# Optimization experiments

Hardware: AMD Instinct MI355X
Metric: run time of the kernel (lower is better)

## Reference

```python
import jax, jax.numpy as jnp
import numpy as np

BATCH = 8
N_CLASSES = 3            # including background
PRE_NMS_LIMIT = 6000
NMS_THRESH = 0.5
SCALE = 512.0
WINDOW = (0.0, 0.0, 512.0, 512.0)   # y1, x1, y2, x2
STD_DEV = np.array([0.1, 0.1, 0.2, 0.2], np.float32)
GROUP_OFFSET = 4096.0    # > image extent; separates (batch, class) groups in NMS

_RATIOS = np.array([0.5, 1.0, 2.0])
_LEVELS = [((128, 128), 4, 8.0), ((64, 64), 8, 16.0), ((32, 32), 16, 32.0), ((16, 16), 32, 64.0)]


def _gen_anchors():
    # faithful port of generate_pyramid_anchors / generate_anchors (anchor_stride=1)
    out = []
    for (fy, fx), stride, scale in _LEVELS:
        s, r = np.meshgrid(np.array([scale]), _RATIOS)
        s, r = s.flatten(), r.flatten()
        heights = s / np.sqrt(r)
        widths = s * np.sqrt(r)
        sy = np.arange(fy) * stride
        sx = np.arange(fx) * stride
        sx, sy = np.meshgrid(sx, sy)
        bw, bcx = np.meshgrid(widths, sx)
        bh, bcy = np.meshgrid(heights, sy)
        centers = np.stack([bcy, bcx], axis=2).reshape(-1, 2)
        sizes = np.stack([bh, bw], axis=2).reshape(-1, 2)
        out.append(np.concatenate([centers - 0.5 * sizes, centers + 0.5 * sizes], axis=1))
    return np.concatenate(out, axis=0).astype(np.float32)  # (65280, 4) yxyx


def setup_inputs() -> dict:
    key = jax.random.key(0)
    k1, k2 = jax.random.split(key)
    anchors = jnp.asarray(_gen_anchors())
    n_anchors = anchors.shape[0]
    n_prop = BATCH * n_anchors
    logits = jax.random.normal(k1, (n_prop, N_CLASSES), jnp.float32)
    probs = jax.nn.softmax(logits, axis=-1)
    deltas = jax.random.normal(k2, (n_prop, 4), jnp.float32)
    batch_ixs = jnp.repeat(jnp.arange(BATCH, dtype=jnp.int64), n_anchors)
    return {"probs": probs, "deltas": deltas, "anchors": anchors, "batch_ixs": batch_ixs}


def _apply_box_deltas_2d(boxes, deltas):
    # boxes: (K,4) yxyx (normalized); deltas: (K,4) dy,dx,dh,dw
    h = boxes[:, 2] - boxes[:, 0]
    w = boxes[:, 3] - boxes[:, 1]
    cy = boxes[:, 0] + 0.5 * h + deltas[:, 0] * h
    cx = boxes[:, 1] + 0.5 * w + deltas[:, 1] * w
    h = h * jnp.exp(deltas[:, 2])
    w = w * jnp.exp(deltas[:, 3])
    y1 = cy - 0.5 * h
    x1 = cx - 0.5 * w
    return jnp.stack([y1, x1, y1 + h, x1 + w], axis=1)


def _nms_keep(boxes, thresh):
    # boxes (K,4), already sorted by score descending; returns bool keep mask.
    y1, x1, y2, x2 = boxes[:, 0], boxes[:, 1], boxes[:, 2], boxes[:, 3]
    areas = (y2 - y1 + 1.0) * (x2 - x1 + 1.0)
    ih = jnp.clip(jnp.minimum(y2[:, None], y2[None, :]) - jnp.maximum(y1[:, None], y1[None, :]) + 1.0, 0.0)
    iw = jnp.clip(jnp.minimum(x2[:, None], x2[None, :]) - jnp.maximum(x1[:, None], x1[None, :]) + 1.0, 0.0)
    inter = ih * iw
    iou = inter / (areas[:, None] + areas[None, :] - inter)  # (K,K)
    K = boxes.shape[0]
    idx = jnp.arange(K)

    def body(i, keep):
        sup = (iou[i] >= thresh) & (idx > i) & keep[i]
        return keep & ~sup

    return jax.lax.fori_loop(0, K, body, jnp.ones((K,), bool))


def reference(probs, deltas, anchors, batch_ixs):
    n_anchors = anchors.shape[0]
    n_fg = probs.shape[1] - 1
    # trim to top pre_nms_limit foreground scores (flat over proposals x fg classes)
    fg = probs[:, 1:].reshape(-1)
    scores, flat_ix = jax.lax.top_k(fg, PRE_NMS_LIMIT)  # sorted descending
    prop_ix = flat_ix // n_fg
    class_ids = flat_ix % n_fg + 1
    b = batch_ixs[prop_ix]
    a = anchors[prop_ix % n_anchors]        # anchors tiled per batch element
    d = deltas[prop_ix] * jnp.asarray(STD_DEV)
    rois = _apply_box_deltas_2d(a / SCALE, d) * SCALE
    lo = jnp.array([WINDOW[0], WINDOW[1], WINDOW[0], WINDOW[1]], rois.dtype)
    hi = jnp.array([WINDOW[2], WINDOW[3], WINDOW[2], WINDOW[3]], rois.dtype)
    rois = jnp.clip(rois, lo, hi)
    # batched per-class NMS: offset boxes so different (batch, class) groups never overlap
    group = (b * (n_fg + 1) + class_ids).astype(rois.dtype) * GROUP_OFFSET
    keep = _nms_keep(rois + group[:, None], NMS_THRESH)
    detections = jnp.concatenate(
        [rois, scores[:, None], keep.astype(rois.dtype)[:, None]], axis=1)  # (K, 6)
    return detections, class_ids, b
```

## Files before the change

kernel.cpp:

```cpp
#include <hip/hip_runtime.h>
#include <math.h>

typedef unsigned int u32;
typedef unsigned short u16;
typedef unsigned long long u64;

#define PRE_NMS 6000
#define NBLK    94
#define KMAX    640
#define MSTRIDE 11
#define MAXW    10
#define MTILE   (MAXW * MAXW)
#define FINEB   8192
#define LOWB    8064
#define NHB     64
#define CANDMAX 16384
#define NGRP    24
#define FLOOR_BITS 0x3F000000u

#define CTR_OFF    0
#define FINEH_OFF  256
#define BCNT_OFF   33024
#define GBITS_OFF  98560
#define ZERO_LEN   (32768 + 65536 + 18432)
#define CAND_OFF   116992
#define BOXR_OFF   248064
#define KG_OFF     344320
#define GRANKG_OFF 344576
#define BOXG_OFF   406016
#define AREAG_OFF  651776
#define MASKG_OFF  713216
#define BASE_OFF   2064896
#define PART_OFF   2130432

__device__ __forceinline__ u32 bucket_of(u32 bits) {
    if (bits >= FLOOR_BITS) {
        u32 fb = (bits - FLOOR_BITS) >> 10; if (fb > FINEB - 1) fb = FINEB - 1;
        return fb;
    }
    return 8192u + (bits >> 17);
}

__global__ __launch_bounds__(1024) void hist_kernel(const float4* __restrict__ probs4,
                                                    u32* __restrict__ fineh,
                                                    u32* __restrict__ partials, int n_prop) {
    __shared__ u32 hf[FINEB];
    __shared__ u32 hl[2][LOWB];
    int t = threadIdx.x;
    for (int i = t; i < FINEB; i += 1024) hf[i] = 0u;
    for (int i = t; i < 2 * LOWB; i += 1024) ((u32*)hl)[i] = 0u;
    __syncthreads();
    u32* l = hl[(t >> 6) & 1];
    int nq = n_prop >> 2;
    int idx = blockIdx.x * 1024 + t;
    int stride = gridDim.x * 1024;
    for (int q = idx; q < nq; q += stride) {
        float4 a = probs4[3 * q + 0];
        float4 b = probs4[3 * q + 1];
        float4 c = probs4[3 * q + 2];
        float vs[8] = {a.y, a.z, b.x, b.y, b.w, c.x, c.z, c.w};
        #pragma unroll
        for (int e = 0; e < 8; ++e) {
            u32 bits = __float_as_uint(vs[e]);
            if (bits >= FLOOR_BITS) {
                u32 fb = (bits - FLOOR_BITS) >> 10; if (fb >= FINEB) fb = FINEB - 1;
                atomicAdd(&hf[fb], 1u);
            } else {
                atomicAdd(&l[bits >> 17], 1u);
            }
        }
    }
    __syncthreads();
    for (int b = t; b < FINEB; b += 1024) {
        u32 v = hf[b];
        if (v) atomicAdd(&fineh[b], v);
    }
    u32* outp = partials + blockIdx.x * LOWB;
    for (int b = t; b < LOWB; b += 1024) outp[b] = hl[0][b] + hl[1][b];
}

__global__ __launch_bounds__(1024) void pivot_kernel(const u32* __restrict__ fineh,
                                                     const u32* __restrict__ partials,
                                                     u32* __restrict__ ctr,
                                                     u32* __restrict__ base) {
    __shared__ u32 fh[FINEB];
    __shared__ u32 sd[1024];
    int t = threadIdx.x;
    if (t == 0) { ctr[0] = 0u; ctr[1] = 0u; }
    for (int b = t; b < FINEB; b += 1024) fh[b] = fineh[b];
    __syncthreads();
    int hi = FINEB - 1 - 8 * t;
    u32 L = 0;
    #pragma unroll
    for (int e = 0; e < 8; ++e) L += fh[hi - e];
    sd[t] = L;
    __syncthreads();
    for (int off = 1; off < 1024; off <<= 1) {
        u32 x = (t >= off) ? sd[t - off] : 0u;
        __syncthreads();
        sd[t] += x;
        __syncthreads();
    }
    u32 incl = sd[t], excl = incl - L;
    u32 fineTotal = sd[1023];
    {
        u32 run = excl;
        #pragma unroll
        for (int e = 0; e < 8; ++e) {
            int fb = hi - e;
            base[fb] = run;
            u32 c = fh[fb];
            if (run < (u32)PRE_NMS && run + c >= (u32)PRE_NMS) {
                ctr[1] = FLOOR_BITS + ((u32)fb << 10);
                u32 m = run + c; if (m > (u32)CANDMAX) m = (u32)CANDMAX;
                ctr[0] = m;
            }
            run += c;
        }
    }
    if (fineTotal >= (u32)PRE_NMS) return;

    u32 rem = (u32)PRE_NMS - fineTotal;
    __syncthreads();
    for (int b = t; b < FINEB; b += 1024) {
        u32 s = 0;
        if (b < LOWB) {
            for (int k = 0; k < NHB; ++k) s += partials[k * LOWB + b];
        }
        fh[b] = s;
    }
    __syncthreads();
    L = 0;
    #pragma unroll
    for (int e = 0; e < 8; ++e) L += fh[hi - e];
    sd[t] = L;
    __syncthreads();
    for (int off = 1; off < 1024; off <<= 1) {
        u32 x = (t >= off) ? sd[t - off] : 0u;
        __syncthreads();
        sd[t] += x;
        __syncthreads();
    }
    incl = sd[t]; excl = incl - L;
    {
        u32 run = excl;
        #pragma unroll
        for (int e = 0; e < 8; ++e) {
            int lb = hi - e;
            base[8192 + lb] = fineTotal + run;
            u32 c = fh[lb];
            if (run < rem && run + c >= rem) {
                ctr[1] = ((u32)lb) << 17;
                u32 m = fineTotal + run + c; if (m > (u32)CANDMAX) m = (u32)CANDMAX;
                ctr[0] = m;
            }
            run += c;
        }
    }
}

__global__ __launch_bounds__(256) void scatter_kernel(const float4* __restrict__ probs4,
                                                      const u32* __restrict__ ctr,
                                                      const u32* __restrict__ base,
                                                      u32* __restrict__ bcnt,
                                                      u64* __restrict__ cand,
                                                      int n_prop) {
    u32 pivot = ctr[1];
    int nq = n_prop >> 2;
    int idx = blockIdx.x * 256 + threadIdx.x;
    int stride = gridDim.x * 256;
    for (int q = idx; q < nq; q += stride) {
        float4 a = probs4[3 * q + 0];
        float4 b = probs4[3 * q + 1];
        float4 c = probs4[3 * q + 2];
        float vs[8] = {a.y, a.z, b.x, b.y, b.w, c.x, c.z, c.w};
        #pragma unroll
        for (int e = 0; e < 8; ++e) {
            u32 bits = __float_as_uint(vs[e]);
            if (bits >= pivot) {
                u32 bk = bucket_of(bits);
                u32 off = atomicAdd(&bcnt[bk], 1u);
                u32 slot = base[bk] + off;
                u32 i = (u32)(8 * q + e);
                if (slot < (u32)CANDMAX) cand[slot] = ((u64)bits << 32) | (u64)(~i);
            }
        }
    }
}

__global__ __launch_bounds__(256) void rankdecode_kernel(const u64* __restrict__ cand,
                                                         const u32* __restrict__ ctr,
                                                         const u32* __restrict__ base,
                                                         const u32* __restrict__ bcnt,
                                                         const float4* __restrict__ deltas4,
                                                         const float4* __restrict__ anchors4,
                                                         float4* __restrict__ boxr,
                                                         u32* __restrict__ gbits,
                                                         float* __restrict__ out,
                                                         int n_anch) {
    u32 M = ctr[0]; if (M > (u32)CANDMAX) M = (u32)CANDMAX;
    u32 i = blockIdx.x * 256 + threadIdx.x;
    if (i >= M) return;
    u64 key = cand[i];
    u32 bits = (u32)(key >> 32);
    u32 bk = bucket_of(bits);
    u32 b0 = base[bk];
    u32 n = bcnt[bk];
    u32 r = b0;
    if (n > 1) {
        u32 end = b0 + n; if (end > M) end = M;
        u32 cnt = 0;
        for (u32 j = b0; j < end; ++j) cnt += (cand[j] > key) ? 1u : 0u;
        r = b0 + cnt;
    }
    if (r >= (u32)PRE_NMS) return;
    u32 flat = ~((u32)key);
    int p = (int)(flat >> 1);
    int cls = (int)(flat & 1u) + 1;
    int b = p / n_anch;
    int g = b * 3 + cls;
    int aidx = p - b * n_anch;
    float score = __uint_as_float(bits);
    float4 a = anchors4[aidx];
    float4 d = deltas4[p];
    float d0 = d.x * 0.1f, d1 = d.y * 0.1f, d2 = d.z * 0.2f, d3 = d.w * 0.2f;
    float y1 = a.x * (1.0f / 512.0f), x1 = a.y * (1.0f / 512.0f);
    float y2 = a.z * (1.0f / 512.0f), x2 = a.w * (1.0f / 512.0f);
    float h = y2 - y1, w = x2 - x1;
    float cy = y1 + 0.5f * h + d0 * h;
    float cx = x1 + 0.5f * w + d1 * w;
    h = h * expf(d2);
    w = w * expf(d3);
    float ry1 = (cy - 0.5f * h) * 512.0f;
    float rx1 = (cx - 0.5f * w) * 512.0f;
    float ry2 = (cy - 0.5f * h + h) * 512.0f;
    float rx2 = (cx - 0.5f * w + w) * 512.0f;
    ry1 = fminf(fmaxf(ry1, 0.0f), 512.0f);
    rx1 = fminf(fmaxf(rx1, 0.0f), 512.0f);
    ry2 = fminf(fmaxf(ry2, 0.0f), 512.0f);
    rx2 = fminf(fmaxf(rx2, 0.0f), 512.0f);
    out[r * 6 + 0] = ry1;
    out[r * 6 + 1] = rx1;
    out[r * 6 + 2] = ry2;
    out[r * 6 + 3] = rx2;
    out[r * 6 + 4] = score;
    out[r * 6 + 5] = 1.0f;
    out[PRE_NMS * 6 + r] = (float)cls;
    out[PRE_NMS * 7 + r] = (float)b;
    boxr[r] = make_float4(ry1, rx1, ry2, rx2);
    atomicOr(&gbits[g * 192 + (r >> 5)], 1u << (r & 31));
}

__global__ __launch_bounds__(512) void prep_kernel(const u32* __restrict__ gbits,
                                                   const float4* __restrict__ boxr,
                                                   u32* __restrict__ kg,
                                                   u32* __restrict__ grankg,
                                                   float4* __restrict__ boxg,
                                                   float* __restrict__ areag) {
    __shared__ int bpre[96];
    __shared__ u16 grankS[KMAX];
    __shared__ int sK;
    int g = blockIdx.x, t = threadIdx.x, lane = t & 63, wv = t >> 6;
    const u32* rb32 = gbits + g * 192;

    if (t < 64) {
        u64 w0 = (u64)rb32[2 * lane] | ((u64)rb32[2 * lane + 1] << 32);
        u64 w1 = (lane < NBLK - 64)
                 ? ((u64)rb32[128 + 2 * lane] | ((u64)rb32[129 + 2 * lane] << 32)) : 0ull;
        int c0 = (int)__popcll(w0), c1 = (int)__popcll(w1);
        int i0 = c0, i1 = c1;
        #pragma unroll
        for (int off = 1; off < 64; off <<= 1) {
            int a = __shfl_up(i0, off); if (lane >= off) i0 += a;
            int b = __shfl_up(i1, off); if (lane >= off) i1 += b;
        }
        int tot0 = __shfl(i0, 63), tot1 = __shfl(i1, 63);
        bpre[lane] = i0 - c0;
        if (lane < 32) bpre[64 + lane] = tot0 + ((lane < NBLK - 64) ? (i1 - c1) : 0);
        if (lane == 0) { sK = tot0 + tot1; kg[g] = (u32)(tot0 + tot1); }
    }
    __syncthreads();
    int K = sK;
    if (K == 0) return;
    int Kc = (K < KMAX) ? K : KMAX;

    for (int blk = wv; blk < NBLK; blk += 8) {
        u64 wmask = (u64)rb32[2 * blk] | ((u64)rb32[2 * blk + 1] << 32);
        if ((wmask >> lane) & 1ull) {
            int pos = bpre[blk] + (int)__popcll(wmask & ((1ull << lane) - 1ull));
            if (pos < KMAX) grankS[pos] = (u16)((blk << 6) | lane);
        }
    }
    __syncthreads();

    float4* bg = boxg + g * KMAX;
    float*  ag = areag + g * KMAX;
    u32*    gr = grankg + g * KMAX;
    for (int m = t; m < KMAX; m += 512) {
        if (m < Kc) {
            int r = grankS[m];
            float4 bb = boxr[r];
            bg[m] = bb;
            ag[m] = (bb.z - bb.x + 1.0f) * (bb.w - bb.y + 1.0f);
            gr[m] = (u32)r;
        } else {
            bg[m] = make_float4(-3e30f, -3e30f, -3e30f, -3e30f);
            ag[m] = 3e38f;
        }
    }
}

__global__ __launch_bounds__(64) void mask_kernel(const u32* __restrict__ kg,
                                                  const float4* __restrict__ boxg,
                                                  const float* __restrict__ areag,
                                                  u64* __restrict__ maskg) {
    int g = blockIdx.y;
    u32 K = kg[g];
    if (K == 0u) return;
    int Kc = (K < (u32)KMAX) ? (int)K : KMAX;
    int W = (Kc + 63) >> 6;
    int u = blockIdx.x;
    int c = u / MAXW, rbk = u % MAXW;
    if (c >= W || rbk >= W) return;
    int lane = threadIdx.x;
    int r = rbk * 64 + lane;
    u64* mg = maskg + (size_t)g * (KMAX * MSTRIDE);
    if (rbk > c) { mg[r * MSTRIDE + c] = 0ull; return; }
    int j0 = c << 6;
    const float4* bg = boxg + g * KMAX;
    const float*  ag = areag + g * KMAX;
    float4 rb = bg[r];
    float  ra = ag[r];
    float4 cb = bg[j0 + lane];
    float  ca = ag[j0 + lane];
    u64 word = 0ull;
    #pragma unroll 8
    for (int q = 0; q < 64; ++q) {
        float cbx = __shfl(cb.x, q);
        float cby = __shfl(cb.y, q);
        float cbz = __shfl(cb.z, q);
        float cbw = __shfl(cb.w, q);
        float cav = __shfl(ca, q);
        float ih = fminf(rb.z, cbz) - fmaxf(rb.x, cbx) + 1.0f;
        float iw = fminf(rb.w, cbw) - fmaxf(rb.y, cby) + 1.0f;
        ih = fmaxf(ih, 0.0f); iw = fmaxf(iw, 0.0f);
        bool o = (3.0f * ih * iw >= ra + cav) && ((j0 + q) > r);
        if (o) word |= (1ull << q);
    }
    mg[r * MSTRIDE + c] = word;
}

__global__ __launch_bounds__(512) void greedy_kernel(const u32* __restrict__ kg,
                                                     const u32* __restrict__ grankg,
                                                     const u64* __restrict__ maskg,
                                                     float* __restrict__ out) {
    __shared__ u64 maskm[KMAX * MSTRIDE + 64];
    __shared__ u16 grank[KMAX];
    int g = blockIdx.x, t = threadIdx.x, lane = t & 63;
    u32 K = kg[g];
    if (K == 0u) return;
    int Kc = (K < (u32)KMAX) ? (int)K : KMAX;
    int W = (Kc + 63) >> 6;
    const u64* mg = maskg + (size_t)g * (KMAX * MSTRIDE);
    int nw = Kc * MSTRIDE;
    for (int m = t; m < nw; m += 512) maskm[m] = mg[m];
    for (int m = nw + t; m < nw + 64; m += 512) maskm[m] = 0ull;
    for (int m = t; m < Kc; m += 512) grank[m] = (u16)grankg[g * KMAX + m];
    __syncthreads();

    if (t >= 64) return;
    u64 remv = 0ull;
    for (int w = 0; w < W; ++w) {
        int r0 = w << 6;
        int rend = Kc - r0; if (rend > 64) rend = 64;
        u64 curw = __shfl(remv, w);
        u64 kb = 0ull;
        for (int b0 = 0; b0 < rend; b0 += 8) {
            int n = rend - b0; if (n > 8) n = 8;
            u64 mrow[8], dg[8];
            #pragma unroll
            for (int j = 0; j < 8; ++j) {
                int rr = r0 + b0 + ((j < n) ? j : 0);
                mrow[j] = maskm[rr * MSTRIDE + lane];
                dg[j]   = maskm[rr * MSTRIDE + w];
            }
            #pragma unroll
            for (int j = 0; j < 8; ++j) {
                if (j < n) {
                    int b = b0 + j;
                    u64 km = ((curw >> b) & 1ull) ? 0ull : ~0ull;
                    curw |= dg[j] & km;
                    remv |= mrow[j] & km;
                    kb |= km & (1ull << b);
                }
            }
        }
        if (lane < rend)
            out[(int)grank[r0 + lane] * 6 + 5] = ((kb >> lane) & 1ull) ? 1.0f : 0.0f;
    }
}

extern "C" void kernel_launch(void* const* d_in, const int* in_sizes, int n_in,
                              void* d_out, int out_size, void* d_ws, size_t ws_size,
                              hipStream_t stream) {
    const float*  probs    = (const float*)d_in[0];
    const float4* deltas4  = (const float4*)d_in[1];
    const float4* anchors4 = (const float4*)d_in[2];
    int n_prop = in_sizes[1] / 4;
    int n_anch = in_sizes[2] / 4;

    char* ws = (char*)d_ws;
    u32* ctr      = (u32*)(ws + CTR_OFF);
    u32* fineh    = (u32*)(ws + FINEH_OFF);
    u32* bcnt     = (u32*)(ws + BCNT_OFF);
    u32* gbits    = (u32*)(ws + GBITS_OFF);
    u64* cand     = (u64*)(ws + CAND_OFF);
    float4* boxr  = (float4*)(ws + BOXR_OFF);
    u32* kg       = (u32*)(ws + KG_OFF);
    u32* grankg   = (u32*)(ws + GRANKG_OFF);
    float4* boxg  = (float4*)(ws + BOXG_OFF);
    float* areag  = (float*)(ws + AREAG_OFF);
    u64* maskg    = (u64*)(ws + MASKG_OFF);
    u32* base     = (u32*)(ws + BASE_OFF);
    u32* partials = (u32*)(ws + PART_OFF);
    float* out    = (float*)d_out;

    hipMemsetAsync(ws + FINEH_OFF, 0, ZERO_LEN, stream);
    hist_kernel<<<NHB, 1024, 0, stream>>>((const float4*)probs, fineh, partials, n_prop);
    pivot_kernel<<<1, 1024, 0, stream>>>(fineh, partials, ctr, base);
    scatter_kernel<<<256, 256, 0, stream>>>((const float4*)probs, ctr, base, bcnt,
                                            cand, n_prop);
    rankdecode_kernel<<<CANDMAX / 256, 256, 0, stream>>>(cand, ctr, base, bcnt,
                                                         deltas4, anchors4,
                                                         boxr, gbits, out, n_anch);
    prep_kernel<<<NGRP, 512, 0, stream>>>(gbits, boxr, kg, grankg, boxg, areag);
    mask_kernel<<<dim3(MTILE, NGRP), 64, 0, stream>>>(kg, boxg, areag, maskg);
    greedy_kernel<<<NGRP, 512, 0, stream>>>(kg, grankg, maskg, out);
}
```

Baseline: 140.1 us.

## Fuse histogram and pivot kernels via last-block ticket; widen hist and scatter grids

Merges the histogram and pivot launches into one kernel. The last block to finish, detected through an atomic ticket counter, performs the pivot prefix-scan, reusing the shared histogram buffers. This removes one kernel launch and its dependency gap. It also doubles the histogram grid and the scatter grid to add parallelism, and widens the memset to zero the counters. The risk is heavier global atomic traffic on fineh and more partial rows for the pivot step to reduce.

After: 145.0 us. +3.5%, slower.

```diff
diff --git a/kernel.cpp b/kernel.cpp
--- a/kernel.cpp
+++ b/kernel.cpp
@@ -13,7 +13,7 @@
 #define MTILE   (MAXW * MAXW)
 #define FINEB   8192
 #define LOWB    8064
-#define NHB     64
+#define NHB     128
 #define CANDMAX 16384
 #define NGRP    24
 #define FLOOR_BITS 0x3F000000u
@@ -22,7 +22,7 @@
 #define FINEH_OFF  256
 #define BCNT_OFF   33024
 #define GBITS_OFF  98560
-#define ZERO_LEN   (32768 + 65536 + 18432)
+#define ZERO_LEN   116992
 #define CAND_OFF   116992
 #define BOXR_OFF   248064
 #define KG_OFF     344320
@@ -41,11 +41,15 @@
     return 8192u + (bits >> 17);
 }
 
-__global__ __launch_bounds__(1024) void hist_kernel(const float4* __restrict__ probs4,
-                                                    u32* __restrict__ fineh,
-                                                    u32* __restrict__ partials, int n_prop) {
+__global__ __launch_bounds__(1024) void histpivot_kernel(const float4* __restrict__ probs4,
+                                                         u32* __restrict__ fineh,
+                                                         u32* __restrict__ partials,
+                                                         u32* __restrict__ ctr,
+                                                         u32* __restrict__ base,
+                                                         int n_prop) {
     __shared__ u32 hf[FINEB];
     __shared__ u32 hl[2][LOWB];
+    __shared__ u32 s_tick;
     int t = threadIdx.x;
     for (int i = t; i < FINEB; i += 1024) hf[i] = 0u;
     for (int i = t; i < 2 * LOWB; i += 1024) ((u32*)hl)[i] = 0u;
@@ -77,16 +81,18 @@
     }
     u32* outp = partials + blockIdx.x * LOWB;
     for (int b = t; b < LOWB; b += 1024) outp[b] = hl[0][b] + hl[1][b];
-}
-
-__global__ __launch_bounds__(1024) void pivot_kernel(const u32* __restrict__ fineh,
-                                                     const u32* __restrict__ partials,
-                                                     u32* __restrict__ ctr,
-                                                     u32* __restrict__ base) {
-    __shared__ u32 fh[FINEB];
-    __shared__ u32 sd[1024];
-    int t = threadIdx.x;
-    if (t == 0) { ctr[0] = 0u; ctr[1] = 0u; }
+    __syncthreads();
+
+    if (t == 0) {
+        __threadfence();
+        s_tick = atomicAdd(&ctr[2], 1u);
+    }
+    __syncthreads();
+    if (s_tick != (u32)gridDim.x - 1u) return;
+
+    __threadfence();
+    u32* fh = hf;
+    u32* sd = hl[0];
     for (int b = t; b < FINEB; b += 1024) fh[b] = fineh[b];
     __syncthreads();
     int hi = FINEB - 1 - 8 * t;
@@ -425,10 +431,10 @@
     u32* partials = (u32*)(ws + PART_OFF);
     float* out    = (float*)d_out;
 
-    hipMemsetAsync(ws + FINEH_OFF, 0, ZERO_LEN, stream);
-    hist_kernel<<<NHB, 1024, 0, stream>>>((const float4*)probs, fineh, partials, n_prop);
-    pivot_kernel<<<1, 1024, 0, stream>>>(fineh, partials, ctr, base);
-    scatter_kernel<<<256, 256, 0, stream>>>((const float4*)probs, ctr, base, bcnt,
+    hipMemsetAsync(ws, 0, ZERO_LEN, stream);
+    histpivot_kernel<<<NHB, 1024, 0, stream>>>((const float4*)probs, fineh, partials,
+                                               ctr, base, n_prop);
+    scatter_kernel<<<512, 256, 0, stream>>>((const float4*)probs, ctr, base, bcnt,
                                             cand, n_prop);
     rankdecode_kernel<<<CANDMAX / 256, 256, 0, stream>>>(cand, ctr, base, bcnt,
                                                          deltas4, anchors4,
```
